# Kernel tuning notes

Measured on AMD Instinct MI355X. Metric: run time of the kernel, lower is better.

The kernel has to match this reference:

```python
import jax, jax.numpy as jnp
import numpy as np

B, T, E = 128, 128, 1024
MD = 50          # mask_dim
H = 256          # per-direction GRU hidden (l_hidden_size=512)
D = 512          # biGRU output dim
CO = 256         # conv output channels
K = 4            # CRF tags (2+2)
NL = 3           # sentiment labels
C1, C2 = 0.1, 0.1


def setup_inputs() -> dict:
    key = jax.random.key(0)
    ks = jax.random.split(key, 16)
    IN = E + MD
    g = lambda k, s, sc=0.05: jax.random.normal(k, s, dtype=jnp.float32) * sc
    z = lambda s: jnp.zeros(s, jnp.float32)
    return {
        "sents": jax.random.normal(ks[0], (B, T, E), dtype=jnp.float32),
        "masks": jax.random.randint(ks[1], (B, T), 0, 2),
        "labels": jax.random.randint(ks[2], (B,), 0, NL),
        "lens": jnp.maximum(jax.random.randint(ks[3], (B,), 1, T + 1), 1),
        "mask_emb": g(ks[4], (2, MD), 1.0),
        "Wih_f": g(ks[5], (3 * H, IN)), "Whh_f": g(ks[6], (3 * H, H)),
        "bih_f": z((3 * H,)), "bhh_f": z((3 * H,)),
        "Wih_b": g(ks[7], (3 * H, IN)), "Whh_b": g(ks[8], (3 * H, H)),
        "bih_b": z((3 * H,)), "bhh_b": z((3 * H,)),
        "conv_w": g(ks[9], (CO, D, 3)), "conv_b": z((CO,)),
        "W_tri": g(ks[10], (K, CO)), "b_tri": z((K,)),
        "transitions": g(ks[11], (K, K), 1.0),
        "W_lab": g(ks[12], (NL, CO)), "b_lab": z((NL,)),
    }


def _gru(xg, mask, Whh, bhh, reverse):
    # xg: [T,B,3H] precomputed input projections; mask: [T,B,1]
    Hh = Whh.shape[1]

    def step(h, inp):
        gg, m = inp
        hg = h @ Whh.T + bhh
        r = jax.nn.sigmoid(gg[:, :Hh] + hg[:, :Hh])
        zt = jax.nn.sigmoid(gg[:, Hh:2 * Hh] + hg[:, Hh:2 * Hh])
        n = jnp.tanh(gg[:, 2 * Hh:] + r * hg[:, 2 * Hh:])
        hn = (1.0 - zt) * n + zt * h
        hn = m * hn + (1.0 - m) * h  # padded steps carry state (packed-seq semantics)
        return hn, hn

    h0 = jnp.zeros((xg.shape[1], Hh), xg.dtype)
    _, hs = jax.lax.scan(step, h0, (xg, mask), reverse=reverse)
    return hs  # [T,B,H]


def reference(sents, masks, labels, lens, mask_emb, Wih_f, Whh_f, bih_f, bhh_f,
              Wih_b, Whh_b, bih_b, bhh_b, conv_w, conv_b, W_tri, b_tri,
              transitions, W_lab, b_lab):
    wm = (jnp.arange(T)[None, :] < lens[:, None]).astype(jnp.float32)  # [B,T]
    # SimpleCatTgtMasked: concat mask embedding
    x = jnp.concatenate([sents, mask_emb[masks]], axis=-1)  # [B,T,E+MD]
    mT = wm.T[:, :, None]  # [T,B,1]
    xg_f = jnp.einsum('btc,gc->tbg', x, Wih_f) + bih_f
    xg_b = jnp.einsum('btc,gc->tbg', x, Wih_b) + bih_b
    hf = _gru(xg_f, mT, Whh_f, bhh_f, False)
    hb = _gru(xg_b, mT, Whh_b, bhh_b, True)
    ctx = jnp.concatenate([hf, hb], axis=-1).transpose(1, 0, 2)  # [B,T,D]
    # Conv1d(D->CO, k=3, pad=1) + ReLU
    c = jax.lax.conv_general_dilated(ctx.transpose(0, 2, 1), conv_w, (1,), ((1, 1),),
                                     dimension_numbers=('NCH', 'OIH', 'NCH'))
    ctx2 = jax.nn.relu(c + conv_b[None, :, None]).transpose(0, 2, 1)  # [B,T,CO]
    feats = jnp.einsum('btc,kc->btk', ctx2, W_tri) + b_tri  # [B,T,K]
    # masked linear-chain CRF forward-backward (log-space)
    fT = feats.transpose(1, 0, 2)  # [T,B,K]
    mS = wm.T[1:, :, None]         # [T-1,B,1]

    def fstep(a, inp):
        f_t, m_t = inp
        an = f_t + jax.nn.logsumexp(a[:, :, None] + transitions[None], axis=1)
        a = m_t * an + (1.0 - m_t) * a
        return a, a

    a0 = fT[0]
    _, alphas = jax.lax.scan(fstep, a0, (fT[1:], mS))
    alpha = jnp.concatenate([a0[None], alphas], axis=0)  # [T,B,K]

    def bstep(b, inp):
        f_n, m_n = inp  # feats/mask at t+1
        bn = jax.nn.logsumexp(transitions[None] + (f_n + b)[:, None, :], axis=2)
        b = m_n * bn + (1.0 - m_n) * b
        return b, b

    b_last = jnp.zeros_like(a0)
    _, betas = jax.lax.scan(bstep, b_last, (fT[1:], mS), reverse=True)
    beta = jnp.concatenate([betas, b_last[None]], axis=0)  # [T,B,K]

    marg = jax.nn.softmax(alpha + beta, axis=-1)  # [T,B,K], = exp(alpha+beta-logZ)
    sp = marg[:, :, 1].T * wm  # [B,T] select polarity, zero past length
    gamma = sp.sum(axis=1) / 2.0
    sent_v = jnp.einsum('bt,btc->bc', sp, ctx2) / gamma[:, None]  # [B,CO]
    scores = sent_v @ W_lab.T + b_lab  # [B,NL]
    logp = jax.nn.log_softmax(scores, axis=1)
    cls_loss = -jnp.mean(logp[jnp.arange(B), labels])
    pena = jax.nn.relu(transitions[1, 0] - transitions[0, 0]) + \
           jax.nn.relu(transitions[0, 1] - transitions[1, 1])
    s_prob_norm = jnp.mean(sp.sum(axis=1))
    norm_pen = C1 * pena + C2 * s_prob_norm
    return jnp.stack([cls_loss, norm_pen])
```

## Files before the change

kernel.cpp:

```cpp
#include <hip/hip_runtime.h>
#include <hip/hip_bf16.h>
#include <math.h>

#define B_ 128
#define T_ 128
#define E_ 1024
#define IN_ 1074
#define H_ 256
#define G3_ 768
#define D_ 512
#define CO_ 256

typedef unsigned int uint_t;
typedef _Float16 v2h __attribute__((ext_vector_type(2)));
typedef _Float16 f16x8 __attribute__((ext_vector_type(8)));
typedef float f32x4 __attribute__((ext_vector_type(4)));


__global__ void k_prep_me(const float* __restrict__ mask_emb,
                          const float* __restrict__ Wf, const float* __restrict__ bf,
                          const float* __restrict__ Wb, const float* __restrict__ bb,
                          float* __restrict__ me) {
    int idx = blockIdx.x * 256 + threadIdx.x;
    if (idx >= 2 * 2 * G3_) return;
    int dir = idx / (2 * G3_);
    int rem = idx % (2 * G3_);
    int m = rem / G3_;
    int g = rem % G3_;
    const float* W = dir ? Wb : Wf;
    const float* bi = dir ? bb : bf;
    float acc = bi[g];
    const float* wrow = W + (size_t)g * IN_ + E_;
    const float* e = mask_emb + m * 50;
    #pragma unroll 10
    for (int c = 0; c < 50; ++c) acc += e[c] * wrow[c];
    me[idx] = acc;
}

__device__ __forceinline__ uint_t pk2(float a, float b) {
    uint_t u0 = (uint_t)__builtin_bit_cast(unsigned short, (_Float16)a);
    uint_t u1 = (uint_t)__builtin_bit_cast(unsigned short, (_Float16)b);
    return u0 | (u1 << 16);
}

__global__ void k_scale(const float* __restrict__ Wf, const float* __restrict__ Wb,
                        float* __restrict__ dq, float* __restrict__ inv) {
    int r = blockIdx.x * 256 + threadIdx.x;
    if (r >= 1536) return;
    int d = r / G3_;
    int g = r % G3_;
    const float* W = (d ? Wb : Wf) + (size_t)g * H_;
    float m = 0.f;
    for (int k = 0; k < H_; ++k) m = fmaxf(m, fabsf(W[k]));
    dq[r] = m / 16129.f;
    inv[r] = (m > 0.f) ? 127.f / m : 0.f;
}

__global__ void k_quant(const float* __restrict__ Wf, const float* __restrict__ Wb,
                        const float* __restrict__ inv, uint_t* __restrict__ wi8) {
    int i = blockIdx.x * 256 + threadIdx.x;
    if (i >= 98304) return;
    int w = i & 3;
    int j = (i >> 2) & 255;
    int rest = i >> 10;
    int p = rest % 3;
    int rest2 = rest / 3;
    int q16 = rest2 & 7;
    int khd = rest2 >> 3;
    int kh = khd & 1;
    int d = khd >> 1;
    int g = p * 256 + j;
    int k0 = kh * 128 + q16 * 16 + w * 4;
    const float* W = (d ? Wb : Wf) + (size_t)g * H_ + k0;
    float iv = inv[d * G3_ + g];
    uint_t u = 0;
    #pragma unroll
    for (int c = 0; c < 4; ++c) {
        int q = __float2int_rn(W[c] * iv);
        q = max(-127, min(127, q));
        u |= ((uint_t)(q & 0xff)) << (8 * c);
    }
    wi8[i] = u;
}

__global__ void k_prep_w2(const float* __restrict__ cw, unsigned short* __restrict__ W2) {
    int i = blockIdx.x * 256 + threadIdx.x;
    if (i >= CO_ * 1536) return;
    int co = i / 1536;
    int k = i % 1536;
    int j = k >> 9;
    int d = k & 511;
    float v = cw[(size_t)co * (D_ * 3) + d * 3 + j];
    W2[i] = __builtin_bit_cast(unsigned short, (_Float16)v);
}

__global__ __launch_bounds__(256) void k_cvt_sents(const float* __restrict__ in,
                                                   uint_t* __restrict__ out) {
    int i = blockIdx.x * 256 + threadIdx.x;
    float4 a = reinterpret_cast<const float4*>(in)[i * 2];
    float4 b = reinterpret_cast<const float4*>(in)[i * 2 + 1];
    uint4 o;
    o.x = pk2(a.x, a.y); o.y = pk2(a.z, a.w);
    o.z = pk2(b.x, b.y); o.w = pk2(b.z, b.w);
    reinterpret_cast<uint4*>(out)[i] = o;
}

__global__ __launch_bounds__(256) void k_cvt_w(const float* __restrict__ Wf,
                                               const float* __restrict__ Wb,
                                               uint_t* __restrict__ out) {
    int i = blockIdx.x * 256 + threadIdx.x;
    if (i >= 1536 * 128) return;
    int n = i >> 7, kq = i & 127;
    int dir = n >= G3_;
    int g = n - dir * G3_;
    const float* src = (dir ? Wb : Wf) + (size_t)g * IN_ + kq * 8;
    float2 a = reinterpret_cast<const float2*>(src)[0];
    float2 b = reinterpret_cast<const float2*>(src)[1];
    float2 c = reinterpret_cast<const float2*>(src)[2];
    float2 d = reinterpret_cast<const float2*>(src)[3];
    uint4 o;
    o.x = pk2(a.x, a.y); o.y = pk2(b.x, b.y);
    o.z = pk2(c.x, c.y); o.w = pk2(d.x, d.y);
    reinterpret_cast<uint4*>(out)[i] = o;
}


__device__ __forceinline__ void gload16(const void* g, void* l) {
    __builtin_amdgcn_global_load_lds(
        (const __attribute__((address_space(1))) void*)g,
        (__attribute__((address_space(3))) void*)l, 16, 0, 0);
}

__global__ __launch_bounds__(256) void k_gemm_mfma(
        const _Float16* __restrict__ A16, const _Float16* __restrict__ W16,
        const float* __restrict__ me, const int* __restrict__ masks,
        float* __restrict__ xgf, float* __restrict__ xgb) {
    __shared__ _Float16 As[4096];
    __shared__ _Float16 Bs[4096];
    const int bid = blockIdx.x;
    const int logical = (bid & 7) * 192 + (bid >> 3);
    const int mt = logical / 12, nt = logical % 12;
    const int bm = mt * 128, bn = nt * 128;
    const int tid = threadIdx.x;
    const int w = tid >> 6, lane = tid & 63;
    const int wr = w >> 1, wc = w & 1;

    const int rl = lane & 15;
    const int kb = (lane >> 4) * 16;
    const int st0 = w, st1 = 4 + w;
    const char* gA0 = (const char*)A16 + (size_t)(bm + st0 * 16 + rl) * 2048 + kb;
    const char* gA1 = (const char*)A16 + (size_t)(bm + st1 * 16 + rl) * 2048 + kb;
    const char* gB0 = (const char*)W16 + (size_t)(bn + st0 * 16 + rl) * 2048 + kb;
    const char* gB1 = (const char*)W16 + (size_t)(bn + st1 * 16 + rl) * 2048 + kb;
    char* lA0 = (char*)As + w * 1024;
    char* lA1 = (char*)As + 4096 + w * 1024;
    char* lB0 = (char*)Bs + w * 1024;
    char* lB1 = (char*)Bs + 4096 + w * 1024;

    f32x4 acc[4][4];
    #pragma unroll
    for (int m = 0; m < 4; ++m)
        #pragma unroll
        for (int n = 0; n < 4; ++n)
            acc[m][n] = (f32x4){0.f, 0.f, 0.f, 0.f};

    for (int kB = 0; kB < 2048; kB += 64) {
        gload16(gA0 + kB, lA0);
        gload16(gA1 + kB, lA1);
        gload16(gB0 + kB, lB0);
        gload16(gB1 + kB, lB1);
        __syncthreads();
        f16x8 af[4], bf[4];
        #pragma unroll
        for (int m = 0; m < 4; ++m)
            af[m] = *reinterpret_cast<const f16x8*>(
                (const char*)As + (wr * 4 + m) * 1024 + lane * 16);
        #pragma unroll
        for (int n = 0; n < 4; ++n)
            bf[n] = *reinterpret_cast<const f16x8*>(
                (const char*)Bs + (wc * 4 + n) * 1024 + lane * 16);
        #pragma unroll
        for (int m = 0; m < 4; ++m)
            #pragma unroll
            for (int n = 0; n < 4; ++n)
                acc[m][n] = __builtin_amdgcn_mfma_f32_16x16x32_f16(
                    af[m], bf[n], acc[m][n], 0, 0, 0);
        __syncthreads();
    }

    const int qr = (lane >> 4) * 4;
    const int cc = lane & 15;
    #pragma unroll
    for (int m = 0; m < 4; ++m) {
        #pragma unroll
        for (int q = 0; q < 4; ++q) {
            const int bt = bm + wr * 64 + m * 16 + qr + q;
            const int mk = masks[bt];
            const int b = bt >> 7, t = bt & 127;
            #pragma unroll
            for (int n = 0; n < 4; ++n) {
                const int col = bn + wc * 64 + n * 16 + cc;
                const int dir = col >= G3_;
                const int g = col - dir * G3_;
                float v = acc[m][n][q] + me[dir * (2 * G3_) + mk * G3_ + g];
                float* dst = (dir ? xgb : xgf) + ((size_t)(t * B_ + b)) * G3_ + g;
                *dst = v;
            }
        }
    }
}

__device__ __forceinline__ int sdot4(uint_t a, uint_t b, int c) {
#if __has_builtin(__builtin_amdgcn_sdot4)
    return __builtin_amdgcn_sdot4((int)a, (int)b, c, false);
#else
    int r = c;
    r += ((int)(a << 24) >> 24) * ((int)(b << 24) >> 24);
    r += ((int)(a << 16) >> 24) * ((int)(b << 16) >> 24);
    r += ((int)(a << 8) >> 24) * ((int)(b << 8) >> 24);
    r += ((int)a >> 24) * ((int)b >> 24);
    return r;
#endif
}

__global__ __launch_bounds__(512, 1) void k_gru(
        const float* __restrict__ xgf, const float* __restrict__ xgb,
        const uint_t* __restrict__ wi8, const float* __restrict__ dq,
        const float* __restrict__ bhhf, const float* __restrict__ bhhb,
        const int* __restrict__ lens, _Float16* __restrict__ ctx16p) {
    const int dir = blockIdx.y;
    const int b = blockIdx.x;
    const int tid = threadIdx.x;
    const int j = tid & 255;
    const int kh = tid >> 8;
    const float* xg = dir ? xgb : xgf;
    const float* bhh = dir ? bhhb : bhhf;
    const uint4* wp4 = (const uint4*)wi8 + (size_t)dir * (2 * 8 * 3 * 256);
    _Float16* c16 = ctx16p + (size_t)b * (T_ + 2) * D_;

    __shared__ uint_t hq_s[64];
    __shared__ int part[3][256];

    c16[tid] = (_Float16)0.f;
    c16[(size_t)(T_ + 1) * D_ + tid] = (_Float16)0.f;

    uint4 w4[3][8];
    #pragma unroll
    for (int q = 0; q < 8; ++q)
        #pragma unroll
        for (int p = 0; p < 3; ++p)
            w4[p][q] = wp4[((size_t)((kh * 8 + q) * 3 + p)) * 256 + j];
    #pragma unroll
    for (int q = 0; q < 8; ++q)
        #pragma unroll
        for (int p = 0; p < 3; ++p)
            asm volatile("" : "+v"(w4[p][q].x), "+v"(w4[p][q].y),
                              "+v"(w4[p][q].z), "+v"(w4[p][q].w));

    if (tid < 64) hq_s[tid] = 0u;
    const int len = lens[b];
    const float dq0 = dq[dir * G3_ + j];
    const float dq1 = dq[dir * G3_ + 256 + j];
    const float dq2 = dq[dir * G3_ + 512 + j];
    const float bh0 = bhh[j], bh1 = bhh[H_ + j], bh2 = bhh[2 * H_ + j];
    float hcur = 0.f;
    float g0 = 0.f, g1 = 0.f, g2 = 0.f;
    int t = dir ? (T_ - 1) : 0;
    if (kh == 0) {
        const float* r = xg + ((size_t)(t * B_ + b)) * G3_;
        g0 = r[j]; g1 = r[H_ + j]; g2 = r[2 * H_ + j];
    }
    __syncthreads();

    for (int s = 0; s < T_; ++s) {
        const int tn = dir ? (T_ - 2 - s) : (s + 1);
        float n0 = 0.f, n1 = 0.f, n2 = 0.f;
        if (kh == 0 && s < T_ - 1) {
            const float* r = xg + ((size_t)(tn * B_ + b)) * G3_;
            n0 = r[j]; n1 = r[H_ + j]; n2 = r[2 * H_ + j];
        }
        int a0 = 0, a1 = 0, a2 = 0;
        const uint4* hv = (const uint4*)hq_s + kh * 8;
        #pragma unroll
        for (int q = 0; q < 8; ++q) {
            uint4 h4 = hv[q];
            a0 = sdot4(w4[0][q].x, h4.x, a0); a0 = sdot4(w4[0][q].y, h4.y, a0);
            a0 = sdot4(w4[0][q].z, h4.z, a0); a0 = sdot4(w4[0][q].w, h4.w, a0);
            a1 = sdot4(w4[1][q].x, h4.x, a1); a1 = sdot4(w4[1][q].y, h4.y, a1);
            a1 = sdot4(w4[1][q].z, h4.z, a1); a1 = sdot4(w4[1][q].w, h4.w, a1);
            a2 = sdot4(w4[2][q].x, h4.x, a2); a2 = sdot4(w4[2][q].y, h4.y, a2);
            a2 = sdot4(w4[2][q].z, h4.z, a2); a2 = sdot4(w4[2][q].w, h4.w, a2);
        }
        if (kh == 1) {
            part[0][j] = a0; part[1][j] = a1; part[2][j] = a2;
        }
        __syncthreads();
        if (kh == 0) {
            float A0 = (float)(a0 + part[0][j]) * dq0;
            float A1 = (float)(a1 + part[1][j]) * dq1;
            float A2 = (float)(a2 + part[2][j]) * dq2;
            float rg = 1.f / (1.f + expf(-(g0 + A0 + bh0)));
            float zg = 1.f / (1.f + expf(-(g1 + A1 + bh1)));
            float ng = tanhf(g2 + rg * (A2 + bh2));
            float v = (1.f - zg) * ng + zg * hcur;
            hcur = (t < len) ? v : hcur;
            c16[(size_t)(t + 1) * D_ + dir * H_ + j] = (_Float16)hcur;
            int qi = __float2int_rn(hcur * 127.f);
            ((signed char*)hq_s)[j] = (signed char)qi;
        }
        __syncthreads();
        g0 = n0; g1 = n1; g2 = n2;
        t = tn;
    }
}

__global__ __launch_bounds__(256) void k_conv_mfma(
        const _Float16* __restrict__ C16, const _Float16* __restrict__ W2,
        const float* __restrict__ cb, float* __restrict__ ctx2) {
    __shared__ _Float16 As[4096];
    __shared__ _Float16 Bs[4096];
    const int b = blockIdx.x >> 1;
    const int nt = blockIdx.x & 1;
    const int bn = nt * 128;
    const int tid = threadIdx.x;
    const int w = tid >> 6, lane = tid & 63;
    const int wr = w >> 1, wc = w & 1;
    const int rl = lane & 15;
    const int kb = (lane >> 4) * 16;
    const char* gA0 = (const char*)C16 + ((size_t)(b * (T_ + 2) + w * 16 + rl)) * 1024 + kb;
    const char* gA1 = (const char*)C16 + ((size_t)(b * (T_ + 2) + 64 + w * 16 + rl)) * 1024 + kb;
    const char* gB0 = (const char*)W2 + (size_t)(bn + w * 16 + rl) * 3072 + kb;
    const char* gB1 = (const char*)W2 + (size_t)(bn + 64 + w * 16 + rl) * 3072 + kb;
    char* lA0 = (char*)As + w * 1024;
    char* lA1 = (char*)As + 4096 + w * 1024;
    char* lB0 = (char*)Bs + w * 1024;
    char* lB1 = (char*)Bs + 4096 + w * 1024;

    f32x4 acc[4][4];
    #pragma unroll
    for (int m = 0; m < 4; ++m)
        #pragma unroll
        for (int n = 0; n < 4; ++n)
            acc[m][n] = (f32x4){0.f, 0.f, 0.f, 0.f};

    for (int kB = 0; kB < 3072; kB += 64) {
        gload16(gA0 + kB, lA0);
        gload16(gA1 + kB, lA1);
        gload16(gB0 + kB, lB0);
        gload16(gB1 + kB, lB1);
        __syncthreads();
        f16x8 af[4], bf[4];
        #pragma unroll
        for (int m = 0; m < 4; ++m)
            af[m] = *reinterpret_cast<const f16x8*>(
                (const char*)As + (wr * 4 + m) * 1024 + lane * 16);
        #pragma unroll
        for (int n = 0; n < 4; ++n)
            bf[n] = *reinterpret_cast<const f16x8*>(
                (const char*)Bs + (wc * 4 + n) * 1024 + lane * 16);
        #pragma unroll
        for (int m = 0; m < 4; ++m)
            #pragma unroll
            for (int n = 0; n < 4; ++n)
                acc[m][n] = __builtin_amdgcn_mfma_f32_16x16x32_f16(
                    af[m], bf[n], acc[m][n], 0, 0, 0);
        __syncthreads();
    }

    const int qr = (lane >> 4) * 4;
    const int cc = lane & 15;
    #pragma unroll
    for (int m = 0; m < 4; ++m) {
        #pragma unroll
        for (int q = 0; q < 4; ++q) {
            const int t = wr * 64 + m * 16 + qr + q;
            #pragma unroll
            for (int n = 0; n < 4; ++n) {
                const int co = bn + wc * 64 + n * 16 + cc;
                float v = acc[m][n][q] + cb[co];
                ctx2[((size_t)(b * T_ + t)) * CO_ + co] = fmaxf(v, 0.f);
            }
        }
    }
}

__global__ __launch_bounds__(256) void k_head(
        const float* __restrict__ ctx2, const float* __restrict__ W_tri,
        const float* __restrict__ b_tri, const float* __restrict__ trans,
        const float* __restrict__ W_lab, const float* __restrict__ b_lab,
        const int* __restrict__ lens, const int* __restrict__ labels,
        float* __restrict__ loss_b, float* __restrict__ spsum_b) {
    const int b = blockIdx.x;
    const int tid = threadIdx.x;
    const int w = tid >> 6, lane = tid & 63;
    __shared__ float f_s[T_][4];
    __shared__ float al[T_][4];
    __shared__ float be[T_][4];
    __shared__ float sp_s[T_];
    __shared__ float sv_s[CO_];
    __shared__ float sred[4];
    __shared__ float s_spsum;
    const int len = lens[b];
    const float* base = ctx2 + (size_t)b * T_ * CO_;

    {
        float wt[4][4];
        #pragma unroll
        for (int k = 0; k < 4; ++k)
            #pragma unroll
            for (int q = 0; q < 4; ++q)
                wt[k][q] = W_tri[k * CO_ + lane + 64 * q];
        float bt0 = b_tri[0], bt1 = b_tri[1], bt2 = b_tri[2], bt3 = b_tri[3];
        for (int t = w; t < T_; t += 4) {
            const float* row = base + (size_t)t * CO_;
            float v0 = row[lane], v1 = row[lane + 64],
                  v2 = row[lane + 128], v3 = row[lane + 192];
            float p0 = v0 * wt[0][0] + v1 * wt[0][1] + v2 * wt[0][2] + v3 * wt[0][3];
            float p1 = v0 * wt[1][0] + v1 * wt[1][1] + v2 * wt[1][2] + v3 * wt[1][3];
            float p2 = v0 * wt[2][0] + v1 * wt[2][1] + v2 * wt[2][2] + v3 * wt[2][3];
            float p3 = v0 * wt[3][0] + v1 * wt[3][1] + v2 * wt[3][2] + v3 * wt[3][3];
            #pragma unroll
            for (int off = 32; off > 0; off >>= 1) {
                p0 += __shfl_xor(p0, off);
                p1 += __shfl_xor(p1, off);
                p2 += __shfl_xor(p2, off);
                p3 += __shfl_xor(p3, off);
            }
            if (lane == 0) {
                f_s[t][0] = p0 + bt0; f_s[t][1] = p1 + bt1;
                f_s[t][2] = p2 + bt2; f_s[t][3] = p3 + bt3;
            }
        }
    }
    __syncthreads();

    if (w == 0 && lane < 4) {
        const int j = lane;
        float tc0 = trans[0 * 4 + j], tc1 = trans[1 * 4 + j],
              tc2 = trans[2 * 4 + j], tc3 = trans[3 * 4 + j];
        float a = f_s[0][j];
        al[0][j] = a;
        for (int t = 1; t < T_; ++t) {
            float a0 = __shfl(a, 0), a1 = __shfl(a, 1),
                  a2 = __shfl(a, 2), a3 = __shfl(a, 3);
            float s0 = a0 + tc0, s1 = a1 + tc1, s2 = a2 + tc2, s3 = a3 + tc3;
            float m = fmaxf(fmaxf(s0, s1), fmaxf(s2, s3));
            float sum = expf(s0 - m) + expf(s1 - m) + expf(s2 - m) + expf(s3 - m);
            float an = f_s[t][j] + m + logf(sum);
            if (t < len) a = an;
            al[t][j] = a;
        }
    } else if (w == 1 && lane < 4) {
        const int i = lane;
        float tr0 = trans[i * 4 + 0], tr1 = trans[i * 4 + 1],
              tr2 = trans[i * 4 + 2], tr3 = trans[i * 4 + 3];
        float bb = 0.f;
        be[T_ - 1][i] = 0.f;
        for (int t = T_ - 2; t >= 0; --t) {
            float b0 = __shfl(bb, 0), b1 = __shfl(bb, 1),
                  b2 = __shfl(bb, 2), b3 = __shfl(bb, 3);
            float s0 = tr0 + f_s[t + 1][0] + b0;
            float s1 = tr1 + f_s[t + 1][1] + b1;
            float s2 = tr2 + f_s[t + 1][2] + b2;
            float s3 = tr3 + f_s[t + 1][3] + b3;
            float m = fmaxf(fmaxf(s0, s1), fmaxf(s2, s3));
            float sum = expf(s0 - m) + expf(s1 - m) + expf(s2 - m) + expf(s3 - m);
            float bn = m + logf(sum);
            if (t + 1 < len) bb = bn;
            be[t][i] = bb;
        }
    }
    __syncthreads();

    if (tid < T_) {
        int t = tid;
        float s0 = al[t][0] + be[t][0];
        float s1 = al[t][1] + be[t][1];
        float s2 = al[t][2] + be[t][2];
        float s3 = al[t][3] + be[t][3];
        float m = fmaxf(fmaxf(s0, s1), fmaxf(s2, s3));
        float e0 = expf(s0 - m), e1 = expf(s1 - m), e2 = expf(s2 - m), e3 = expf(s3 - m);
        float p1 = e1 / (e0 + e1 + e2 + e3);
        sp_s[t] = (t < len) ? p1 : 0.f;
    }
    __syncthreads();
    if (w == 0) {
        float s = sp_s[lane] + sp_s[lane + 64];
        #pragma unroll
        for (int off = 32; off > 0; off >>= 1) s += __shfl_xor(s, off);
        if (lane == 0) s_spsum = s;
    }
    __syncthreads();
    const float spsum = s_spsum;

    {
        float acc0 = 0.f, acc1 = 0.f, acc2 = 0.f, acc3 = 0.f;
        #pragma unroll 2
        for (int t = 0; t < T_; t += 4) {
            acc0 += sp_s[t + 0] * base[(size_t)(t + 0) * CO_ + tid];
            acc1 += sp_s[t + 1] * base[(size_t)(t + 1) * CO_ + tid];
            acc2 += sp_s[t + 2] * base[(size_t)(t + 2) * CO_ + tid];
            acc3 += sp_s[t + 3] * base[(size_t)(t + 3) * CO_ + tid];
        }
        sv_s[tid] = (acc0 + acc1 + acc2 + acc3) * 2.f / spsum;
    }
    __syncthreads();

    if (w < 3) {
        const float* wl = W_lab + w * CO_;
        float p = sv_s[lane] * wl[lane] + sv_s[lane + 64] * wl[lane + 64]
                + sv_s[lane + 128] * wl[lane + 128] + sv_s[lane + 192] * wl[lane + 192];
        #pragma unroll
        for (int off = 32; off > 0; off >>= 1) p += __shfl_xor(p, off);
        if (lane == 0) sred[w] = p + b_lab[w];
    }
    __syncthreads();
    if (tid == 0) {
        float m = fmaxf(sred[0], fmaxf(sred[1], sred[2]));
        float lse = m + logf(expf(sred[0] - m) + expf(sred[1] - m) + expf(sred[2] - m));
        loss_b[b] = lse - sred[labels[b]];
        spsum_b[b] = spsum;
    }
}

__global__ void k_final(const float* __restrict__ loss_b, const float* __restrict__ spsum_b,
                        const float* __restrict__ trans, float* __restrict__ out) {
    __shared__ float s1[128], s2[128];
    int tid = threadIdx.x;
    s1[tid] = loss_b[tid];
    s2[tid] = spsum_b[tid];
    __syncthreads();
    for (int off = 64; off > 0; off >>= 1) {
        if (tid < off) { s1[tid] += s1[tid + off]; s2[tid] += s2[tid + off]; }
        __syncthreads();
    }
    if (tid == 0) {
        float pena = fmaxf(trans[1 * 4 + 0] - trans[0 * 4 + 0], 0.f)
                   + fmaxf(trans[0 * 4 + 1] - trans[1 * 4 + 1], 0.f);
        out[0] = s1[0] / (float)B_;
        out[1] = 0.1f * pena + 0.1f * (s2[0] / (float)B_);
    }
}

extern "C" void kernel_launch(void* const* d_in, const int* in_sizes, int n_in,
                              void* d_out, int out_size, void* d_ws, size_t ws_size,
                              hipStream_t stream) {
    const float* sents   = (const float*)d_in[0];
    const int*   masks   = (const int*)d_in[1];
    const int*   labels  = (const int*)d_in[2];
    const int*   lens    = (const int*)d_in[3];
    const float* mask_emb= (const float*)d_in[4];
    const float* Wih_f   = (const float*)d_in[5];
    const float* Whh_f   = (const float*)d_in[6];
    const float* bih_f   = (const float*)d_in[7];
    const float* bhh_f   = (const float*)d_in[8];
    const float* Wih_b   = (const float*)d_in[9];
    const float* Whh_b   = (const float*)d_in[10];
    const float* bih_b   = (const float*)d_in[11];
    const float* bhh_b   = (const float*)d_in[12];
    const float* conv_w  = (const float*)d_in[13];
    const float* conv_b  = (const float*)d_in[14];
    const float* W_tri   = (const float*)d_in[15];
    const float* b_tri   = (const float*)d_in[16];
    const float* trans   = (const float*)d_in[17];
    const float* W_lab   = (const float*)d_in[18];
    const float* b_lab   = (const float*)d_in[19];
    float* out = (float*)d_out;
    float* ws = (float*)d_ws;

    const size_t o_xgf  = 0;
    const size_t o_xgb  = o_xgf  + (size_t)B_ * T_ * G3_;
    const size_t o_ctx  = o_xgb  + (size_t)B_ * T_ * G3_;
    const size_t o_ctx2 = o_ctx  + (size_t)B_ * T_ * D_;
    const size_t o_wp   = o_ctx2 + (size_t)B_ * T_ * CO_;
    const size_t o_me   = o_wp   + (size_t)2 * 32 * 3 * 256 * 4;
    const size_t o_w2   = o_me   + 2 * 2 * G3_;
    const size_t o_lossb= o_w2   + (size_t)D_ * 3 * CO_;
    const size_t o_spsum= o_lossb + B_;

    float* xgf  = ws + o_xgf;
    float* xgb  = ws + o_xgb;
    float* ctx  = ws + o_ctx;
    float* ctx2 = ws + o_ctx2;
    uint_t* wi8 = (uint_t*)(ws + o_wp);
    float* dq   = ws + o_wp + 98304;
    float* invs = ws + o_wp + 98304 + 1536;
    float* me   = ws + o_me;
    unsigned short* W2 = (unsigned short*)(ws + o_w2);
    float* lossb = ws + o_lossb;
    float* spsumb = ws + o_spsum;

    _Float16* sents16 = (_Float16*)ctx;
    _Float16* ctx16p = (_Float16*)ctx;
    _Float16* W16 = (_Float16*)ctx2;

    k_prep_me<<<12, 256, 0, stream>>>(mask_emb, Wih_f, bih_f, Wih_b, bih_b, me);
    k_scale<<<6, 256, 0, stream>>>(Whh_f, Whh_b, dq, invs);
    k_quant<<<384, 256, 0, stream>>>(Whh_f, Whh_b, invs, wi8);
    k_prep_w2<<<1536, 256, 0, stream>>>(conv_w, W2);
    k_cvt_sents<<<8192, 256, 0, stream>>>(sents, (uint_t*)sents16);
    k_cvt_w<<<768, 256, 0, stream>>>(Wih_f, Wih_b, (uint_t*)W16);
    k_gemm_mfma<<<1536, 256, 0, stream>>>(sents16, W16, me, masks, xgf, xgb);
    k_gru<<<dim3(B_, 2), 512, 0, stream>>>(xgf, xgb, wi8, dq, bhh_f, bhh_b, lens, ctx16p);
    k_conv_mfma<<<256, 256, 0, stream>>>(ctx16p, (const _Float16*)W2, conv_b, ctx2);
    k_head<<<128, 256, 0, stream>>>(ctx2, W_tri, b_tri, trans, W_lab, b_lab,
                                    lens, labels, lossb, spsumb);
    k_final<<<1, 128, 0, stream>>>(lossb, spsumb, trans, out);
}
```

Baseline: 392.7 us.

## Store GRU input projections in fp16 and split recurrent weights across registers, LDS, global

The GEMM now writes the precomputed GRU input gates as fp16 instead of fp32, halving the write and per-step read traffic of the xg buffers. The GRU kernel no longer keeps all 24 uint4 weight fragments in registers. Two q-slices stay in registers, 14 fragments are staged in LDS (112 KB), and 4 are re-read from global/L2 every step. This is meant to lower register pressure and spills, at the cost of LDS reads and global loads inside the serial time loop, plus fp16 rounding of the gate inputs.

```diff
diff --git a/kernel.cpp b/kernel.cpp
--- a/kernel.cpp
+++ b/kernel.cpp
@@ -134,7 +134,7 @@
 __global__ __launch_bounds__(256) void k_gemm_mfma(
         const _Float16* __restrict__ A16, const _Float16* __restrict__ W16,
         const float* __restrict__ me, const int* __restrict__ masks,
-        float* __restrict__ xgf, float* __restrict__ xgb) {
+        _Float16* __restrict__ xgf, _Float16* __restrict__ xgb) {
     __shared__ _Float16 As[4096];
     __shared__ _Float16 Bs[4096];
     const int bid = blockIdx.x;
@@ -203,8 +203,8 @@
                 const int dir = col >= G3_;
                 const int g = col - dir * G3_;
                 float v = acc[m][n][q] + me[dir * (2 * G3_) + mk * G3_ + g];
-                float* dst = (dir ? xgb : xgf) + ((size_t)(t * B_ + b)) * G3_ + g;
-                *dst = v;
+                _Float16* dst = (dir ? xgb : xgf) + ((size_t)(t * B_ + b)) * G3_ + g;
+                *dst = (_Float16)v;
             }
         }
     }
@@ -223,8 +223,16 @@
 #endif
 }
 
+__device__ __forceinline__ int dot16(uint4 w, uint4 h, int acc) {
+    acc = sdot4(w.x, h.x, acc);
+    acc = sdot4(w.y, h.y, acc);
+    acc = sdot4(w.z, h.z, acc);
+    acc = sdot4(w.w, h.w, acc);
+    return acc;
+}
+
 __global__ __launch_bounds__(512, 1) void k_gru(
-        const float* __restrict__ xgf, const float* __restrict__ xgb,
+        const _Float16* __restrict__ xgf, const _Float16* __restrict__ xgb,
         const uint_t* __restrict__ wi8, const float* __restrict__ dq,
         const float* __restrict__ bhhf, const float* __restrict__ bhhb,
         const int* __restrict__ lens, _Float16* __restrict__ ctx16p) {
@@ -233,29 +241,43 @@
     const int tid = threadIdx.x;
     const int j = tid & 255;
     const int kh = tid >> 8;
-    const float* xg = dir ? xgb : xgf;
+    const _Float16* xg = dir ? xgb : xgf;
     const float* bhh = dir ? bhhb : bhhf;
     const uint4* wp4 = (const uint4*)wi8 + (size_t)dir * (2 * 8 * 3 * 256);
     _Float16* c16 = ctx16p + (size_t)b * (T_ + 2) * D_;
 
+    __shared__ uint4 wl[14 * 512];
     __shared__ uint_t hq_s[64];
     __shared__ int part[3][256];
 
     c16[tid] = (_Float16)0.f;
     c16[(size_t)(T_ + 1) * D_ + tid] = (_Float16)0.f;
 
-    uint4 w4[3][8];
-    #pragma unroll
-    for (int q = 0; q < 8; ++q)
-        #pragma unroll
-        for (int p = 0; p < 3; ++p)
-            w4[p][q] = wp4[((size_t)((kh * 8 + q) * 3 + p)) * 256 + j];
-    #pragma unroll
-    for (int q = 0; q < 8; ++q)
-        #pragma unroll
-        for (int p = 0; p < 3; ++p)
-            asm volatile("" : "+v"(w4[p][q].x), "+v"(w4[p][q].y),
-                              "+v"(w4[p][q].z), "+v"(w4[p][q].w));
+    #pragma unroll
+    for (int s = 0; s < 12; ++s) {
+        const int q = 2 + s / 3, p = s % 3;
+        wl[s * 512 + tid] = wp4[((size_t)((kh * 8 + q) * 3 + p)) * 256 + j];
+    }
+    #pragma unroll
+    for (int p = 0; p < 2; ++p)
+        wl[(12 + p) * 512 + tid] = wp4[((size_t)((kh * 8 + 6) * 3 + p)) * 256 + j];
+
+    uint4 wr0[3], wr1[3];
+    #pragma unroll
+    for (int p = 0; p < 3; ++p) {
+        wr0[p] = wp4[((size_t)((kh * 8 + 0) * 3 + p)) * 256 + j];
+        wr1[p] = wp4[((size_t)((kh * 8 + 1) * 3 + p)) * 256 + j];
+    }
+    #pragma unroll
+    for (int p = 0; p < 3; ++p) {
+        asm volatile("" : "+v"(wr0[p].x), "+v"(wr0[p].y), "+v"(wr0[p].z), "+v"(wr0[p].w));
+        asm volatile("" : "+v"(wr1[p].x), "+v"(wr1[p].y), "+v"(wr1[p].z), "+v"(wr1[p].w));
+    }
+
+    const uint4* pv62 = wp4 + ((size_t)((kh * 8 + 6) * 3 + 2)) * 256 + j;
+    const uint4* pv70 = wp4 + ((size_t)((kh * 8 + 7) * 3 + 0)) * 256 + j;
+    const uint4* pv71 = wp4 + ((size_t)((kh * 8 + 7) * 3 + 1)) * 256 + j;
+    const uint4* pv72 = wp4 + ((size_t)((kh * 8 + 7) * 3 + 2)) * 256 + j;
 
     if (tid < 64) hq_s[tid] = 0u;
     const int len = lens[b];
@@ -267,30 +289,44 @@
     float g0 = 0.f, g1 = 0.f, g2 = 0.f;
     int t = dir ? (T_ - 1) : 0;
     if (kh == 0) {
-        const float* r = xg + ((size_t)(t * B_ + b)) * G3_;
-        g0 = r[j]; g1 = r[H_ + j]; g2 = r[2 * H_ + j];
-    }
-    __syncthreads();
-
+        const _Float16* r = xg + ((size_t)(t * B_ + b)) * G3_;
+        g0 = (float)r[j]; g1 = (float)r[H_ + j]; g2 = (float)r[2 * H_ + j];
+    }
+    __syncthreads();
+
+    const uint4* hq4 = (const uint4*)hq_s;
     for (int s = 0; s < T_; ++s) {
         const int tn = dir ? (T_ - 2 - s) : (s + 1);
         float n0 = 0.f, n1 = 0.f, n2 = 0.f;
         if (kh == 0 && s < T_ - 1) {
-            const float* r = xg + ((size_t)(tn * B_ + b)) * G3_;
-            n0 = r[j]; n1 = r[H_ + j]; n2 = r[2 * H_ + j];
-        }
+            const _Float16* r = xg + ((size_t)(tn * B_ + b)) * G3_;
+            n0 = (float)r[j]; n1 = (float)r[H_ + j]; n2 = (float)r[2 * H_ + j];
+        }
+        uint4 t62 = *pv62;
+        uint4 t70 = *pv70;
+        uint4 t71 = *pv71;
+        uint4 t72 = *pv72;
+        uint4 hv[8];
+        #pragma unroll
+        for (int q = 0; q < 8; ++q) hv[q] = hq4[kh * 8 + q];
         int a0 = 0, a1 = 0, a2 = 0;
-        const uint4* hv = (const uint4*)hq_s + kh * 8;
-        #pragma unroll
-        for (int q = 0; q < 8; ++q) {
-            uint4 h4 = hv[q];
-            a0 = sdot4(w4[0][q].x, h4.x, a0); a0 = sdot4(w4[0][q].y, h4.y, a0);
-            a0 = sdot4(w4[0][q].z, h4.z, a0); a0 = sdot4(w4[0][q].w, h4.w, a0);
-            a1 = sdot4(w4[1][q].x, h4.x, a1); a1 = sdot4(w4[1][q].y, h4.y, a1);
-            a1 = sdot4(w4[1][q].z, h4.z, a1); a1 = sdot4(w4[1][q].w, h4.w, a1);
-            a2 = sdot4(w4[2][q].x, h4.x, a2); a2 = sdot4(w4[2][q].y, h4.y, a2);
-            a2 = sdot4(w4[2][q].z, h4.z, a2); a2 = sdot4(w4[2][q].w, h4.w, a2);
-        }
+        a0 = dot16(wr0[0], hv[0], a0); a1 = dot16(wr0[1], hv[0], a1); a2 = dot16(wr0[2], hv[0], a2);
+        a0 = dot16(wr1[0], hv[1], a0); a1 = dot16(wr1[1], hv[1], a1); a2 = dot16(wr1[2], hv[1], a2);
+        #pragma unroll
+        for (int ss = 0; ss < 12; ++ss) {
+            const int q = 2 + ss / 3, p = ss % 3;
+            uint4 wv = wl[ss * 512 + tid];
+            if (p == 0) a0 = dot16(wv, hv[q], a0);
+            else if (p == 1) a1 = dot16(wv, hv[q], a1);
+            else a2 = dot16(wv, hv[q], a2);
+        }
+        a0 = dot16(wl[12 * 512 + tid], hv[6], a0);
+        a1 = dot16(wl[13 * 512 + tid], hv[6], a1);
+        a2 = dot16(t62, hv[6], a2);
+        a0 = dot16(t70, hv[7], a0);
+        a1 = dot16(t71, hv[7], a1);
+        a2 = dot16(t72, hv[7], a2);
+
         if (kh == 1) {
             part[0][j] = a0; part[1][j] = a1; part[2][j] = a2;
         }
@@ -507,9 +543,9 @@
     __syncthreads();
 
     if (w < 3) {
-        const float* wl = W_lab + w * CO_;
-        float p = sv_s[lane] * wl[lane] + sv_s[lane + 64] * wl[lane + 64]
-                + sv_s[lane + 128] * wl[lane + 128] + sv_s[lane + 192] * wl[lane + 192];
+        const float* wl_ = W_lab + w * CO_;
+        float p = sv_s[lane] * wl_[lane] + sv_s[lane + 64] * wl_[lane + 64]
+                + sv_s[lane + 128] * wl_[lane + 128] + sv_s[lane + 192] * wl_[lane + 192];
         #pragma unroll
         for (int off = 32; off > 0; off >>= 1) p += __shfl_xor(p, off);
         if (lane == 0) sred[w] = p + b_lab[w];
@@ -578,8 +614,8 @@
     const size_t o_lossb= o_w2   + (size_t)D_ * 3 * CO_;
     const size_t o_spsum= o_lossb + B_;
 
-    float* xgf  = ws + o_xgf;
-    float* xgb  = ws + o_xgb;
+    _Float16* xgf16 = (_Float16*)(ws + o_xgf);
+    _Float16* xgb16 = (_Float16*)(ws + o_xgb);
     float* ctx  = ws + o_ctx;
     float* ctx2 = ws + o_ctx2;
     uint_t* wi8 = (uint_t*)(ws + o_wp);
@@ -600,8 +636,8 @@
     k_prep_w2<<<1536, 256, 0, stream>>>(conv_w, W2);
     k_cvt_sents<<<8192, 256, 0, stream>>>(sents, (uint_t*)sents16);
     k_cvt_w<<<768, 256, 0, stream>>>(Wih_f, Wih_b, (uint_t*)W16);
-    k_gemm_mfma<<<1536, 256, 0, stream>>>(sents16, W16, me, masks, xgf, xgb);
-    k_gru<<<dim3(B_, 2), 512, 0, stream>>>(xgf, xgb, wi8, dq, bhh_f, bhh_b, lens, ctx16p);
+    k_gemm_mfma<<<1536, 256, 0, stream>>>(sents16, W16, me, masks, xgf16, xgb16);
+    k_gru<<<dim3(B_, 2), 512, 0, stream>>>(xgf16, xgb16, wi8, dq, bhh_f, bhh_b, lens, ctx16p);
     k_conv_mfma<<<256, 256, 0, stream>>>(ctx16p, (const _Float16*)W2, conv_b, ctx2);
     k_head<<<128, 256, 0, stream>>>(ctx2, W_tri, b_tri, trans, W_lab, b_lab,
                                     lens, labels, lossb, spsumb);
```

Result: slower. 420.8 us (+7.2%).
